# Kernel optimization log

Hardware: AMD Instinct MI355X
Metric: run time of the kernel (lower is better)

The kernel has to match this reference:

```python
import jax, jax.numpy as jnp
import numpy as np

B, S, T, H, E = 256, 512, 16, 1024, 512  # batch, src_len, trg_steps, hidden, emb_dim


def setup_inputs() -> dict:
    key = jax.random.key(0)
    ks = jax.random.split(key, 10)
    rn = lambda k, sh: jax.random.normal(k, sh, dtype=jnp.float32) * 0.05
    return {
        "trg_emb": rn(ks[0], (B, T, E)),
        "h0": rn(ks[1], (B, H)),
        "c0": rn(ks[2], (B, H)),
        "ctx": rn(ks[3], (B, S, H)),
        "src_len": jax.random.randint(ks[4], (B,), 1, S + 1, dtype=jnp.int32),
        "W_ih": rn(ks[5], (4 * H, E + H)),  # input-feeding: lstm in = emb + hidden
        "W_hh": rn(ks[6], (4 * H, H)),
        "b_ih": jnp.zeros((4 * H,), jnp.float32),
        "b_hh": jnp.zeros((4 * H,), jnp.float32),
        "W_in": rn(ks[7], (H, H)),    # attention linear_in (no bias)
        "W_out": rn(ks[8], (H, 2 * H)),  # attention linear_out (no bias)
    }


def reference(trg_emb, h0, c0, ctx, src_len, W_ih, W_hh, b_ih, b_hh, W_in, W_out):
    # mask[b, s] = s < src_len[b]
    mask = jnp.arange(S)[None, :] < src_len[:, None]  # (B, S)
    neg = jnp.float32(-1e9)

    def step(carry, emb_t):
        h, c, h_tilde = carry  # each (B, H); emb_t (B, E)
        # input feeding: concat target embedding with previous attentional vector
        x = jnp.concatenate([emb_t, h_tilde], axis=1)  # (B, E+H)
        gates = x @ W_ih.T + b_ih + h @ W_hh.T + b_hh  # (B, 4H), pytorch gate order i,f,g,o
        i, f, g, o = jnp.split(gates, 4, axis=1)
        i = jax.nn.sigmoid(i); f = jax.nn.sigmoid(f)
        g = jnp.tanh(g);       o = jax.nn.sigmoid(o)
        c = f * c + i * g
        h = o * jnp.tanh(c)
        # Luong soft-dot attention with src_len masking
        target = h @ W_in.T                                # (B, H)
        scores = jnp.einsum('bsh,bh->bs', ctx, target)     # (B, S)
        scores = jnp.where(mask, scores, neg)
        attn = jax.nn.softmax(scores, axis=-1)
        weighted = jnp.einsum('bs,bsh->bh', attn, ctx)     # (B, H)
        h_tilde = jnp.tanh(jnp.concatenate([weighted, h], axis=1) @ W_out.T)
        return (h, c, h_tilde), h_tilde

    # initial h_tilde = init_hidden[0] (per the original code)
    (h_f, c_f, _), hs = jax.lax.scan(step, (h0, c0, h0), jnp.swapaxes(trg_emb, 0, 1))
    output = jnp.swapaxes(hs, 0, 1)  # (B, T, H)
    return output, h_f, c_f
```

## Files before the change

kernel.cpp:

```cpp
#include <hip/hip_runtime.h>
#include <cstdint>
#include <cstddef>


#define B_ 256
#define S_ 512
#define T_ 16
#define H_ 1024
#define E_ 512
#define NBUF 4

typedef unsigned short u16;
using short8 = __attribute__((ext_vector_type(8))) short;
using f32x4  = __attribute__((ext_vector_type(4))) float;

__device__ __forceinline__ float bf2f(u16 u) {
  union { uint32_t i; float f; } v; v.i = ((uint32_t)u) << 16; return v.f;
}
__device__ __forceinline__ u16 f2bf(float f) {
  union { uint32_t i; float f; } v; v.f = f;
  uint32_t r = v.i + 0x7fffu + ((v.i >> 16) & 1u);
  return (u16)(r >> 16);
}
__device__ __forceinline__ ushort4 cvt4bf(float4 v) {
  ushort4 o; o.x = f2bf(v.x); o.y = f2bf(v.y); o.z = f2bf(v.z); o.w = f2bf(v.w);
  return o;
}
__device__ __forceinline__ float sigmoidf_(float x) { return 1.f / (1.f + __expf(-x)); }

__device__ __forceinline__ void gload_lds16(const void* g, void* l) {
  __builtin_amdgcn_global_load_lds(
      (const __attribute__((address_space(1))) void*)g,
      (__attribute__((address_space(3))) void*)l, 16, 0, 0);
}

struct Reg3 { const u16* A; int lda; const u16* B; int ldb; int kt; };

template <int EPI>
__global__ __launch_bounds__(128) void gemm_k(Reg3 r0, Reg3 r1, Reg3 r2,
                                              int nmb,
                                              float* __restrict__ Cf,
                                              u16* __restrict__ Cb,
                                              const float* __restrict__ bsum,
                                              float* __restrict__ cst,
                                              float* __restrict__ h32o,
                                              u16* __restrict__ hbfo,
                                              const int tstep) {
  __shared__ u16 smA[NBUF][64 * 64];
  __shared__ u16 smB[NBUF][64 * 64];
  const int tid = threadIdx.x;
  const int lane = tid & 63;
  const int wave = tid >> 6;
  const int m0 = (blockIdx.x % nmb) * 64;
  const int n0 = (blockIdx.x / nmb) * 64;
  const int row16 = lane & 15;
  const int kg = lane >> 4;
  const int nt = r0.kt + r1.kt + r2.kt;

  auto stage = [&](int ti, int buf) {
    const int k01 = r0.kt + r1.kt;
    const u16* Ap = (ti < r0.kt) ? r0.A : (ti < k01) ? r1.A : r2.A;
    const u16* Bp = (ti < r0.kt) ? r0.B : (ti < k01) ? r1.B : r2.B;
    const int lda = (ti < r0.kt) ? r0.lda : (ti < k01) ? r1.lda : r2.lda;
    const int ldb = (ti < r0.kt) ? r0.ldb : (ti < k01) ? r1.ldb : r2.ldb;
    const int base = (ti < r0.kt) ? 0 : (ti < k01) ? r0.kt : k01;
    const int kr = (ti - base) << 6;
#pragma unroll
    for (int j = 0; j < 4; ++j) {
      const int c = j * 128 + tid;
      const int row = c >> 3, q = c & 7;
      gload_lds16(Ap + (size_t)(m0 + row) * lda + kr + ((q ^ (row & 7)) << 3),
                  (char*)&smA[buf][0] + (size_t)(j * 128 + wave * 64) * 16);
    }
#pragma unroll
    for (int j = 0; j < 4; ++j) {
      const int c = j * 128 + tid;
      const int row = c >> 3, q = c & 7;
      gload_lds16(Bp + (size_t)(n0 + row) * ldb + kr + ((q ^ (row & 7)) << 3),
                  (char*)&smB[buf][0] + (size_t)(j * 128 + wave * 64) * 16);
    }
  };

  f32x4 acc[4][2] = {};
  stage(0, 0);
  if (nt > 1) stage(1, 1);
  for (int ti = 0; ti < nt; ++ti) {
    const int buf = ti & 3;
    if (ti + 2 < nt) {
      stage(ti + 2, (ti + 2) & 3);
      asm volatile("s_waitcnt vmcnt(16)" ::: "memory");
    } else if (ti + 1 < nt) {
      asm volatile("s_waitcnt vmcnt(8)" ::: "memory");
    } else {
      asm volatile("s_waitcnt vmcnt(0)" ::: "memory");
    }
    __builtin_amdgcn_s_barrier();
    __builtin_amdgcn_sched_barrier(0);
#pragma unroll
    for (int ks = 0; ks < 2; ++ks) {
      short8 af[4], bfr[2];
#pragma unroll
      for (int mi = 0; mi < 4; ++mi) {
        const int R = mi * 16 + row16;
        af[mi] = *(const short8*)((const char*)&smA[buf][0] +
                                  (size_t)(((R << 3) | ((ks * 4 + kg) ^ (R & 7))) << 4));
      }
#pragma unroll
      for (int ni = 0; ni < 2; ++ni) {
        const int R = wave * 32 + ni * 16 + row16;
        bfr[ni] = *(const short8*)((const char*)&smB[buf][0] +
                                   (size_t)(((R << 3) | ((ks * 4 + kg) ^ (R & 7))) << 4));
      }
      asm volatile("s_waitcnt lgkmcnt(0)" ::: "memory");
      __builtin_amdgcn_sched_barrier(0);
#pragma unroll
      for (int mi = 0; mi < 4; ++mi)
#pragma unroll
        for (int ni = 0; ni < 2; ++ni)
          acc[mi][ni] = __builtin_amdgcn_mfma_f32_16x16x32_bf16(af[mi], bfr[ni], acc[mi][ni], 0, 0, 0);
      __builtin_amdgcn_sched_barrier(0);
    }
  }
#pragma unroll
  for (int mi = 0; mi < 4; ++mi) {
#pragma unroll
    for (int ni = 0; ni < 2; ++ni) {
#pragma unroll
      for (int r = 0; r < 4; ++r) {
        const int row = m0 + mi * 16 + (kg << 2) + r;
        const int col = n0 + wave * 32 + ni * 16 + row16;
        float v = acc[mi][ni][r];
        if (EPI == 1) {
          Cb[row * H_ + col] = f2bf(v);
        } else if (EPI == 2) {
          float tv = tanhf(v);
          Cf[(size_t)row * (T_ * H_) + (size_t)tstep * H_ + col] = tv;
          Cb[row * H_ + col] = f2bf(tv);
        } else {
          v += bsum[col];
          float v1 = __shfl_xor(v, 1);
          float v2 = __shfl_xor(v, 2);
          float v3 = __shfl_xor(v, 3);
          if ((lane & 3) == 0) {
            const int u = col >> 2;
            float iv = sigmoidf_(v);
            float fv = sigmoidf_(v1);
            float gv = tanhf(v2);
            float ov = sigmoidf_(v3);
            float cn = fv * cst[row * H_ + u] + iv * gv;
            float hn = ov * tanhf(cn);
            cst[row * H_ + u] = cn;
            h32o[row * H_ + u] = hn;
            hbfo[row * H_ + u] = f2bf(hn);
          }
        }
      }
    }
  }
}

__device__ __forceinline__ int fidx(int lane, int j) {
  return (j << 6) + ((lane + (j << 2)) & 63);
}

__global__ __launch_bounds__(1024) void attn_k(const u16* __restrict__ tgt,
                                               const u16* __restrict__ ctxc,
                                               const int* __restrict__ offs,
                                               const int* __restrict__ src_len,
                                               u16* __restrict__ wwbf) {
  __shared__ float facc[8][1024];
  __shared__ float fm[16], fl[16];
  const int b = blockIdx.x;
  const int tid = threadIdx.x;
  const int lane = tid & 63;
  const int wave = tid >> 6;
  const int len = src_len[b];
  const u16* cb = ctxc + ((size_t)offs[b] << 10);

  float tg[16];
  {
    const u16* tp = tgt + b * H_ + lane * 16;
    short8 v1 = *(const short8*)tp;
    short8 v2 = *(const short8*)(tp + 8);
#pragma unroll
    for (int j = 0; j < 8; ++j) { tg[j] = bf2f((u16)v1[j]); tg[8 + j] = bf2f((u16)v2[j]); }
  }

  float m = -1e30f, l = 0.f;
  float acc[16];
#pragma unroll
  for (int j = 0; j < 16; ++j) acc[j] = 0.f;

  for (int s = wave; s < len; s += 16) {
    const u16* cr = cb + ((size_t)s << 10) + (lane << 4);
    short8 v1 = *(const short8*)cr;
    short8 v2 = *(const short8*)(cr + 8);
    float cf[16];
#pragma unroll
    for (int j = 0; j < 8; ++j) { cf[j] = bf2f((u16)v1[j]); cf[8 + j] = bf2f((u16)v2[j]); }
    float x = 0.f;
#pragma unroll
    for (int j = 0; j < 16; ++j) x += cf[j] * tg[j];
#pragma unroll
    for (int off = 1; off < 64; off <<= 1) x += __shfl_xor(x, off);
    if (x > m) {
      float sc_ = __expf(m - x);
      l *= sc_;
#pragma unroll
      for (int j = 0; j < 16; ++j) acc[j] *= sc_;
      m = x;
    }
    float p = __expf(x - m);
    l += p;
#pragma unroll
    for (int j = 0; j < 16; ++j) acc[j] += p * cf[j];
  }

  if (wave >= 8) {
#pragma unroll
    for (int j = 0; j < 16; ++j) facc[wave - 8][fidx(lane, j)] = acc[j];
    if (lane == 0) { fm[wave] = m; fl[wave] = l; }
  }
  __syncthreads();
  if (wave < 8) {
    float pm = fm[8 + wave];
    float pl = fl[8 + wave];
    float M = fmaxf(m, pm);
    float e1 = __expf(m - M);
    float e2 = __expf(pm - M);
#pragma unroll
    for (int j = 0; j < 16; ++j) {
      float pv = facc[wave][fidx(lane, j)];
      facc[wave][fidx(lane, j)] = acc[j] * e1 + pv * e2;
    }
    if (lane == 0) { fm[wave] = M; fl[wave] = l * e1 + pl * e2; }
  }
  __syncthreads();
  float mstar = -1e30f;
#pragma unroll
  for (int w = 0; w < 8; ++w) mstar = fmaxf(mstar, fm[w]);
  float lsum = 0.f, asum = 0.f;
  const int ri = fidx(tid >> 4, tid & 15);
#pragma unroll
  for (int w = 0; w < 8; ++w) {
    float e = __expf(fm[w] - mstar);
    lsum += fl[w] * e;
    asum += facc[w][ri] * e;
  }
  wwbf[b * H_ + tid] = f2bf(asum / lsum);
}

__global__ __launch_bounds__(256) void scan_k(const int* __restrict__ len,
                                              int* __restrict__ offs) {
  __shared__ int tmp[256];
  const int tid = threadIdx.x;
  const int v = len[tid];
  tmp[tid] = v;
  __syncthreads();
  for (int off = 1; off < 256; off <<= 1) {
    int t = (tid >= off) ? tmp[tid - off] : 0;
    __syncthreads();
    tmp[tid] += t;
    __syncthreads();
  }
  offs[tid] = tmp[tid] - v;
}

__global__ __launch_bounds__(256) void ctx_compact(const float* __restrict__ ctx,
                                                   const int* __restrict__ src_len,
                                                   const int* __restrict__ offs,
                                                   u16* __restrict__ ctxc) {
  const int b = blockIdx.x;
  const int n4 = src_len[b] << 8;
  const float4* s = (const float4*)(ctx + ((size_t)b << 19));
  ushort4* d = (ushort4*)(ctxc + ((size_t)offs[b] << 10));
  for (int i = threadIdx.x; i < n4; i += 256) d[i] = cvt4bf(s[i]);
}

__global__ __launch_bounds__(256) void convert_all(
    const float* __restrict__ W_ih, const float* __restrict__ W_hh,
    const float* __restrict__ W_in, const float* __restrict__ W_out,
    const float* __restrict__ trg_emb,
    const float* __restrict__ b_ih, const float* __restrict__ b_hh,
    const float* __restrict__ h0, const float* __restrict__ c0,
    u16* __restrict__ wWih, u16* __restrict__ wWhh, u16* __restrict__ wWin,
    u16* __restrict__ wWout, u16* __restrict__ wemb,
    float* __restrict__ wbsum, u16* __restrict__ wh0, u16* __restrict__ whtbf,
    float* __restrict__ wc) {
  const int gtid = blockIdx.x * 256 + threadIdx.x;
  const int GSZ = 1024 * 256;
  for (int i = gtid; i < 1572864; i += GSZ) {
    const int r = i / 384, c4 = i - r * 384;
    const int rp = ((r & 1023) << 2) + (r >> 10);
    ((ushort4*)wWih)[(size_t)rp * 384 + c4] = cvt4bf(((const float4*)W_ih)[i]);
  }
  for (int i = gtid; i < 1048576; i += GSZ) {
    const int r = i >> 8, c4 = i & 255;
    const int rp = ((r & 1023) << 2) + (r >> 10);
    ((ushort4*)wWhh)[(size_t)rp * 256 + c4] = cvt4bf(((const float4*)W_hh)[i]);
  }
  for (int i = gtid; i < 262144; i += GSZ)
    ((ushort4*)wWin)[i] = cvt4bf(((const float4*)W_in)[i]);
  for (int i = gtid; i < 524288; i += GSZ)
    ((ushort4*)wWout)[i] = cvt4bf(((const float4*)W_out)[i]);
  for (int i = gtid; i < 524288; i += GSZ)
    ((ushort4*)wemb)[i] = cvt4bf(((const float4*)trg_emb)[i]);
  if (gtid < 4096) {
    const int cp = ((gtid & 1023) << 2) + (gtid >> 10);
    wbsum[cp] = b_ih[gtid] + b_hh[gtid];
  }
  for (int i = gtid; i < 262144; i += GSZ) {
    u16 hb = f2bf(h0[i]);
    wh0[i] = hb;
    whtbf[i] = hb;
    wc[i] = c0[i];
  }
}

extern "C" void kernel_launch(void* const* d_in, const int* in_sizes, int n_in,
                              void* d_out, int out_size, void* d_ws, size_t ws_size,
                              hipStream_t stream) {
  const float* trg_emb = (const float*)d_in[0];
  const float* h0      = (const float*)d_in[1];
  const float* c0      = (const float*)d_in[2];
  const float* ctx     = (const float*)d_in[3];
  const int*   src_len = (const int*)d_in[4];
  const float* W_ih    = (const float*)d_in[5];
  const float* W_hh    = (const float*)d_in[6];
  const float* b_ih    = (const float*)d_in[7];
  const float* b_hh    = (const float*)d_in[8];
  const float* W_in    = (const float*)d_in[9];
  const float* W_out   = (const float*)d_in[10];
  float* out = (float*)d_out;

  char* w = (char*)d_ws;
  size_t off = 0;
  auto alloc = [&](size_t bytes) { char* p = w + off; off += bytes; return p; };
  u16*   wWih  = (u16*)  alloc(12582912);
  u16*   wWhh  = (u16*)  alloc(8388608);
  u16*   wWin  = (u16*)  alloc(2097152);
  u16*   wWout = (u16*)  alloc(4194304);
  u16*   wemb  = (u16*)  alloc(4194304);
  float* wbsum = (float*)alloc(16384);
  float* wh32  = (float*)alloc(1048576);
  float* wc    = (float*)alloc(1048576);
  u16*   wh0   = (u16*)  alloc(524288);
  u16*   wh1   = (u16*)  alloc(524288);
  u16*   whtbf = (u16*)  alloc(524288);
  u16*   wtgt  = (u16*)  alloc(524288);
  u16*   wwbf  = (u16*)  alloc(524288);
  int*   woffs = (int*)  alloc(1024);
  u16*   wctxc = (u16*)  alloc(268435456);
  (void)ws_size;

  scan_k<<<dim3(1), dim3(256), 0, stream>>>(src_len, woffs);
  convert_all<<<dim3(1024), dim3(256), 0, stream>>>(
      W_ih, W_hh, W_in, W_out, trg_emb, b_ih, b_hh, h0, c0,
      wWih, wWhh, wWin, wWout, wemb, wbsum, wh0, whtbf, wc);
  ctx_compact<<<dim3(B_), dim3(256), 0, stream>>>(ctx, src_len, woffs, wctxc);

  Reg3 rz = { nullptr, 0, nullptr, 0, 0 };
  for (int t = 0; t < T_; ++t) {
    const u16* hcur = (t & 1) ? wh1 : wh0;
    u16* hnxt = (t & 1) ? wh0 : wh1;
    Reg3 g0 = { wemb + (size_t)t * E_, T_ * E_, wWih,      E_ + H_, 8 };
    Reg3 g1 = { whtbf,                 H_,      wWih + E_, E_ + H_, 16 };
    Reg3 g2 = { hcur,                  H_,      wWhh,      H_,      16 };
    gemm_k<3><<<dim3(256), dim3(128), 0, stream>>>(
        g0, g1, g2, 4, nullptr, nullptr, wbsum, wc, wh32, hnxt, 0);
    Reg3 i0 = { hnxt, H_, wWin, H_, 16 };
    gemm_k<1><<<dim3(64), dim3(128), 0, stream>>>(
        i0, rz, rz, 4, nullptr, wtgt, nullptr, nullptr, nullptr, nullptr, 0);
    attn_k<<<dim3(B_), dim3(1024), 0, stream>>>(wtgt, wctxc, woffs, src_len, wwbf);
    Reg3 o0 = { wwbf, H_, wWout,      2 * H_, 16 };
    Reg3 o1 = { hnxt, H_, wWout + H_, 2 * H_, 16 };
    gemm_k<2><<<dim3(64), dim3(128), 0, stream>>>(
        o0, o1, rz, 4, out, whtbf, nullptr, nullptr, nullptr, nullptr, t);
  }
  hipMemcpyAsync(out + (size_t)B_ * T_ * H_, wh32, (size_t)B_ * H_ * sizeof(float),
                 hipMemcpyDeviceToDevice, stream);
  hipMemcpyAsync(out + (size_t)B_ * T_ * H_ + B_ * H_, wc, (size_t)B_ * H_ * sizeof(float),
                 hipMemcpyDeviceToDevice, stream);
}
```

Before: 2.096 ms.

## Split attention across block pairs, deepen GEMM pipeline, fuse setup kernels

The GEMM kernel now runs four waves in a 2x2 layout with a six-buffer, four-deep prefetch, so more waves share each 64x64 tile. Attention is split across two 512-thread blocks per batch row, each handling half the source positions. The two halves merge their online-softmax partials through a global flag handoff, and if the flag never arrives the first block processes the second half itself. The prefix scan and ctx compaction are folded into the conversion kernel, and the final h/c copies are replaced by writes from the last-step epilogue. This adds spin-wait synchronisation between blocks and reuses pacc across steps, which relies on stream ordering between launches.

Measured after the change: 1.914 ms. -8.7%, faster.

```diff
diff --git a/kernel.cpp b/kernel.cpp
--- a/kernel.cpp
+++ b/kernel.cpp
@@ -8,7 +8,7 @@
 #define T_ 16
 #define H_ 1024
 #define E_ 512
-#define NBUF 4
+#define NBUF 6
 
 typedef unsigned short u16;
 using short8 = __attribute__((ext_vector_type(8))) short;
@@ -37,20 +37,21 @@
 struct Reg3 { const u16* A; int lda; const u16* B; int ldb; int kt; };
 
 template <int EPI>
-__global__ __launch_bounds__(128) void gemm_k(Reg3 r0, Reg3 r1, Reg3 r2,
+__global__ __launch_bounds__(256) void gemm_k(Reg3 r0, Reg3 r1, Reg3 r2,
                                               int nmb,
                                               float* __restrict__ Cf,
                                               u16* __restrict__ Cb,
                                               const float* __restrict__ bsum,
                                               float* __restrict__ cst,
-                                              float* __restrict__ h32o,
                                               u16* __restrict__ hbfo,
+                                              float* __restrict__ outHC,
                                               const int tstep) {
-  __shared__ u16 smA[NBUF][64 * 64];
-  __shared__ u16 smB[NBUF][64 * 64];
+  __shared__ u16 smA[NBUF][4096];
+  __shared__ u16 smB[NBUF][4096];
   const int tid = threadIdx.x;
   const int lane = tid & 63;
   const int wave = tid >> 6;
+  const int wm = wave >> 1, wn = wave & 1;
   const int m0 = (blockIdx.x % nmb) * 64;
   const int n0 = (blockIdx.x / nmb) * 64;
   const int row16 = lane & 15;
@@ -66,31 +67,37 @@
     const int base = (ti < r0.kt) ? 0 : (ti < k01) ? r0.kt : k01;
     const int kr = (ti - base) << 6;
 #pragma unroll
-    for (int j = 0; j < 4; ++j) {
-      const int c = j * 128 + tid;
+    for (int j = 0; j < 2; ++j) {
+      const int c = j * 256 + tid;
       const int row = c >> 3, q = c & 7;
       gload_lds16(Ap + (size_t)(m0 + row) * lda + kr + ((q ^ (row & 7)) << 3),
-                  (char*)&smA[buf][0] + (size_t)(j * 128 + wave * 64) * 16);
-    }
-#pragma unroll
-    for (int j = 0; j < 4; ++j) {
-      const int c = j * 128 + tid;
+                  (char*)&smA[buf][0] + (size_t)(j * 256 + wave * 64) * 16);
+    }
+#pragma unroll
+    for (int j = 0; j < 2; ++j) {
+      const int c = j * 256 + tid;
       const int row = c >> 3, q = c & 7;
       gload_lds16(Bp + (size_t)(n0 + row) * ldb + kr + ((q ^ (row & 7)) << 3),
-                  (char*)&smB[buf][0] + (size_t)(j * 128 + wave * 64) * 16);
+                  (char*)&smB[buf][0] + (size_t)(j * 256 + wave * 64) * 16);
     }
   };
 
-  f32x4 acc[4][2] = {};
+  f32x4 acc[2][2] = {};
   stage(0, 0);
   if (nt > 1) stage(1, 1);
+  if (nt > 2) stage(2, 2);
+  if (nt > 3) stage(3, 3);
   for (int ti = 0; ti < nt; ++ti) {
-    const int buf = ti & 3;
-    if (ti + 2 < nt) {
-      stage(ti + 2, (ti + 2) & 3);
+    const int buf = ti % NBUF;
+    if (ti + 4 < nt) {
+      stage(ti + 4, (ti + 4) % NBUF);
       asm volatile("s_waitcnt vmcnt(16)" ::: "memory");
+    } else if (ti + 3 < nt) {
+      asm volatile("s_waitcnt vmcnt(12)" ::: "memory");
+    } else if (ti + 2 < nt) {
+      asm volatile("s_waitcnt vmcnt(8)" ::: "memory");
     } else if (ti + 1 < nt) {
-      asm volatile("s_waitcnt vmcnt(8)" ::: "memory");
+      asm volatile("s_waitcnt vmcnt(4)" ::: "memory");
     } else {
       asm volatile("s_waitcnt vmcnt(0)" ::: "memory");
     }
@@ -98,23 +105,23 @@
     __builtin_amdgcn_sched_barrier(0);
 #pragma unroll
     for (int ks = 0; ks < 2; ++ks) {
-      short8 af[4], bfr[2];
-#pragma unroll
-      for (int mi = 0; mi < 4; ++mi) {
-        const int R = mi * 16 + row16;
+      short8 af[2], bfr[2];
+#pragma unroll
+      for (int mi = 0; mi < 2; ++mi) {
+        const int R = wm * 32 + mi * 16 + row16;
         af[mi] = *(const short8*)((const char*)&smA[buf][0] +
                                   (size_t)(((R << 3) | ((ks * 4 + kg) ^ (R & 7))) << 4));
       }
 #pragma unroll
       for (int ni = 0; ni < 2; ++ni) {
-        const int R = wave * 32 + ni * 16 + row16;
+        const int R = wn * 32 + ni * 16 + row16;
         bfr[ni] = *(const short8*)((const char*)&smB[buf][0] +
                                    (size_t)(((R << 3) | ((ks * 4 + kg) ^ (R & 7))) << 4));
       }
       asm volatile("s_waitcnt lgkmcnt(0)" ::: "memory");
       __builtin_amdgcn_sched_barrier(0);
 #pragma unroll
-      for (int mi = 0; mi < 4; ++mi)
+      for (int mi = 0; mi < 2; ++mi)
 #pragma unroll
         for (int ni = 0; ni < 2; ++ni)
           acc[mi][ni] = __builtin_amdgcn_mfma_f32_16x16x32_bf16(af[mi], bfr[ni], acc[mi][ni], 0, 0, 0);
@@ -122,13 +129,13 @@
     }
   }
 #pragma unroll
-  for (int mi = 0; mi < 4; ++mi) {
+  for (int mi = 0; mi < 2; ++mi) {
 #pragma unroll
     for (int ni = 0; ni < 2; ++ni) {
 #pragma unroll
       for (int r = 0; r < 4; ++r) {
-        const int row = m0 + mi * 16 + (kg << 2) + r;
-        const int col = n0 + wave * 32 + ni * 16 + row16;
+        const int row = m0 + wm * 32 + mi * 16 + (kg << 2) + r;
+        const int col = n0 + wn * 32 + ni * 16 + row16;
         float v = acc[mi][ni][r];
         if (EPI == 1) {
           Cb[row * H_ + col] = f2bf(v);
@@ -150,8 +157,11 @@
             float cn = fv * cst[row * H_ + u] + iv * gv;
             float hn = ov * tanhf(cn);
             cst[row * H_ + u] = cn;
-            h32o[row * H_ + u] = hn;
             hbfo[row * H_ + u] = f2bf(hn);
+            if (outHC) {
+              outHC[row * H_ + u] = hn;
+              outHC[B_ * H_ + row * H_ + u] = cn;
+            }
           }
         }
       }
@@ -163,35 +173,39 @@
   return (j << 6) + ((lane + (j << 2)) & 63);
 }
 
-__global__ __launch_bounds__(1024) void attn_k(const u16* __restrict__ tgt,
-                                               const u16* __restrict__ ctxc,
-                                               const int* __restrict__ offs,
-                                               const int* __restrict__ src_len,
-                                               u16* __restrict__ wwbf) {
-  __shared__ float facc[8][1024];
-  __shared__ float fm[16], fl[16];
-  const int b = blockIdx.x;
+__global__ __launch_bounds__(512, 4) void attn_pair(const u16* __restrict__ tgt,
+                                                    const u16* __restrict__ ctxc,
+                                                    const int* __restrict__ woffs,
+                                                    const int* __restrict__ src_len,
+                                                    u16* __restrict__ wwbf,
+                                                    float* __restrict__ pacc,
+                                                    float* __restrict__ pml,
+                                                    int* __restrict__ flag) {
+  __shared__ float facc[7][1024];
+  __shared__ float fm[8], fl[8];
+  const int p = blockIdx.x >> 1;
+  const int half = blockIdx.x & 1;
   const int tid = threadIdx.x;
   const int lane = tid & 63;
   const int wave = tid >> 6;
-  const int len = src_len[b];
-  const u16* cb = ctxc + ((size_t)offs[b] << 10);
+  const int len = src_len[p];
+  const int len2 = (len + 1) >> 1;
+  const u16* cb = ctxc + ((size_t)woffs[p] << 10);
 
   float tg[16];
   {
-    const u16* tp = tgt + b * H_ + lane * 16;
+    const u16* tp = tgt + p * H_ + lane * 16;
     short8 v1 = *(const short8*)tp;
     short8 v2 = *(const short8*)(tp + 8);
 #pragma unroll
     for (int j = 0; j < 8; ++j) { tg[j] = bf2f((u16)v1[j]); tg[8 + j] = bf2f((u16)v2[j]); }
   }
-
   float m = -1e30f, l = 0.f;
   float acc[16];
 #pragma unroll
   for (int j = 0; j < 16; ++j) acc[j] = 0.f;
 
-  for (int s = wave; s < len; s += 16) {
+  auto process = [&](int s) {
     const u16* cr = cb + ((size_t)s << 10) + (lane << 4);
     short8 v1 = *(const short8*)cr;
     short8 v2 = *(const short8*)(cr + 8);
@@ -210,84 +224,102 @@
       for (int j = 0; j < 16; ++j) acc[j] *= sc_;
       m = x;
     }
-    float p = __expf(x - m);
-    l += p;
-#pragma unroll
-    for (int j = 0; j < 16; ++j) acc[j] += p * cf[j];
-  }
-
-  if (wave >= 8) {
-#pragma unroll
-    for (int j = 0; j < 16; ++j) facc[wave - 8][fidx(lane, j)] = acc[j];
+    float pv = __expf(x - m);
+    l += pv;
+#pragma unroll
+    for (int j = 0; j < 16; ++j) acc[j] += pv * cf[j];
+  };
+
+  const int lo = half ? len2 : 0;
+  const int hi = half ? len : len2;
+  for (int s = lo + wave; s < hi; s += 8) process(s);
+
+  if (wave >= 1) {
+#pragma unroll
+    for (int j = 0; j < 16; ++j) facc[wave - 1][fidx(lane, j)] = acc[j];
     if (lane == 0) { fm[wave] = m; fl[wave] = l; }
   }
   __syncthreads();
-  if (wave < 8) {
-    float pm = fm[8 + wave];
-    float pl = fl[8 + wave];
-    float M = fmaxf(m, pm);
-    float e1 = __expf(m - M);
-    float e2 = __expf(pm - M);
-#pragma unroll
-    for (int j = 0; j < 16; ++j) {
-      float pv = facc[wave][fidx(lane, j)];
-      facc[wave][fidx(lane, j)] = acc[j] * e1 + pv * e2;
-    }
-    if (lane == 0) { fm[wave] = M; fl[wave] = l * e1 + pl * e2; }
-  }
-  __syncthreads();
-  float mstar = -1e30f;
-#pragma unroll
-  for (int w = 0; w < 8; ++w) mstar = fmaxf(mstar, fm[w]);
-  float lsum = 0.f, asum = 0.f;
-  const int ri = fidx(tid >> 4, tid & 15);
-#pragma unroll
-  for (int w = 0; w < 8; ++w) {
-    float e = __expf(fm[w] - mstar);
-    lsum += fl[w] * e;
-    asum += facc[w][ri] * e;
-  }
-  wwbf[b * H_ + tid] = f2bf(asum / lsum);
-}
-
-__global__ __launch_bounds__(256) void scan_k(const int* __restrict__ len,
-                                              int* __restrict__ offs) {
-  __shared__ int tmp[256];
-  const int tid = threadIdx.x;
-  const int v = len[tid];
-  tmp[tid] = v;
-  __syncthreads();
-  for (int off = 1; off < 256; off <<= 1) {
-    int t = (tid >= off) ? tmp[tid - off] : 0;
-    __syncthreads();
-    tmp[tid] += t;
-    __syncthreads();
-  }
-  offs[tid] = tmp[tid] - v;
-}
-
-__global__ __launch_bounds__(256) void ctx_compact(const float* __restrict__ ctx,
-                                                   const int* __restrict__ src_len,
-                                                   const int* __restrict__ offs,
-                                                   u16* __restrict__ ctxc) {
-  const int b = blockIdx.x;
-  const int n4 = src_len[b] << 8;
-  const float4* s = (const float4*)(ctx + ((size_t)b << 19));
-  ushort4* d = (ushort4*)(ctxc + ((size_t)offs[b] << 10));
-  for (int i = threadIdx.x; i < n4; i += 256) d[i] = cvt4bf(s[i]);
+  if (wave == 0) {
+#pragma unroll
+    for (int w = 1; w < 8; ++w) {
+      float pm2 = fm[w], pl2 = fl[w];
+      float M = fmaxf(m, pm2);
+      float e1 = __expf(m - M), e2 = __expf(pm2 - M);
+#pragma unroll
+      for (int j = 0; j < 16; ++j)
+        acc[j] = acc[j] * e1 + facc[w - 1][fidx(lane, j)] * e2;
+      l = l * e1 + pl2 * e2;
+      m = M;
+    }
+    if (half == 1) {
+      float* pa = pacc + (size_t)p * 1024;
+#pragma unroll
+      for (int j4 = 0; j4 < 4; ++j4) {
+        float4 v;
+        v.x = acc[j4 * 4]; v.y = acc[j4 * 4 + 1];
+        v.z = acc[j4 * 4 + 2]; v.w = acc[j4 * 4 + 3];
+        *(float4*)&pa[lane * 16 + j4 * 4] = v;
+      }
+      if (lane == 0) { pml[2 * p] = m; pml[2 * p + 1] = l; }
+      asm volatile("s_waitcnt vmcnt(0)" ::: "memory");
+      if (lane == 0)
+        __hip_atomic_store(flag + p, 1, __ATOMIC_RELEASE, __HIP_MEMORY_SCOPE_AGENT);
+    } else {
+      int got = 0;
+      if (lane == 0) {
+        for (unsigned c2 = 0; c2 < (1u << 10); ++c2) {
+          if (__hip_atomic_load(flag + p, __ATOMIC_RELAXED, __HIP_MEMORY_SCOPE_AGENT) != 0) {
+            got = 1; break;
+          }
+          __builtin_amdgcn_s_sleep(2);
+        }
+        if (got)
+          (void)__hip_atomic_load(flag + p, __ATOMIC_ACQUIRE, __HIP_MEMORY_SCOPE_AGENT);
+      }
+      got = __shfl(got, 0);
+      if (got) {
+        const float* pa = pacc + (size_t)p * 1024;
+        float pm2 = pml[2 * p], pl2 = pml[2 * p + 1];
+        float M = fmaxf(m, pm2);
+        float e1 = __expf(m - M), e2 = __expf(pm2 - M);
+#pragma unroll
+        for (int j = 0; j < 16; ++j)
+          acc[j] = acc[j] * e1 + pa[lane * 16 + j] * e2;
+        l = l * e1 + pl2 * e2;
+        m = M;
+      } else {
+        for (int s = len2; s < len; ++s) process(s);
+      }
+      const float inv = 1.f / l;
+#pragma unroll
+      for (int j4 = 0; j4 < 4; ++j4) {
+        ushort4 o;
+        o.x = f2bf(acc[j4 * 4] * inv);
+        o.y = f2bf(acc[j4 * 4 + 1] * inv);
+        o.z = f2bf(acc[j4 * 4 + 2] * inv);
+        o.w = f2bf(acc[j4 * 4 + 3] * inv);
+        *(ushort4*)(wwbf + p * H_ + lane * 16 + j4 * 4) = o;
+      }
+    }
+  }
 }
 
 __global__ __launch_bounds__(256) void convert_all(
     const float* __restrict__ W_ih, const float* __restrict__ W_hh,
     const float* __restrict__ W_in, const float* __restrict__ W_out,
-    const float* __restrict__ trg_emb,
+    const float* __restrict__ trg_emb, const float* __restrict__ ctx,
     const float* __restrict__ b_ih, const float* __restrict__ b_hh,
     const float* __restrict__ h0, const float* __restrict__ c0,
+    const int* __restrict__ src_len,
     u16* __restrict__ wWih, u16* __restrict__ wWhh, u16* __restrict__ wWin,
     u16* __restrict__ wWout, u16* __restrict__ wemb,
     float* __restrict__ wbsum, u16* __restrict__ wh0, u16* __restrict__ whtbf,
-    float* __restrict__ wc) {
-  const int gtid = blockIdx.x * 256 + threadIdx.x;
+    float* __restrict__ wc, int* __restrict__ woffs, u16* __restrict__ ctxc) {
+  __shared__ int tmp[256];
+  const int bid = blockIdx.x;
+  const int tid = threadIdx.x;
+  const int gtid = bid * 256 + tid;
   const int GSZ = 1024 * 256;
   for (int i = gtid; i < 1572864; i += GSZ) {
     const int r = i / 384, c4 = i - r * 384;
@@ -314,6 +346,21 @@
     wh0[i] = hb;
     whtbf[i] = hb;
     wc[i] = c0[i];
+  }
+  if (bid >= 768) {
+    const int b = bid - 768;
+    tmp[tid] = (tid < b) ? src_len[tid] : 0;
+    __syncthreads();
+    for (int o = 128; o > 0; o >>= 1) {
+      if (tid < o) tmp[tid] += tmp[tid + o];
+      __syncthreads();
+    }
+    const int off = tmp[0];
+    if (tid == 0) woffs[b] = off;
+    const int n4 = src_len[b] << 8;
+    const float4* s = (const float4*)(ctx + ((size_t)b << 19));
+    ushort4* d = (ushort4*)(ctxc + ((size_t)off << 10));
+    for (int i = tid; i < n4; i += 256) d[i] = cvt4bf(s[i]);
   }
 }
 
@@ -342,7 +389,6 @@
   u16*   wWout = (u16*)  alloc(4194304);
   u16*   wemb  = (u16*)  alloc(4194304);
   float* wbsum = (float*)alloc(16384);
-  float* wh32  = (float*)alloc(1048576);
   float* wc    = (float*)alloc(1048576);
   u16*   wh0   = (u16*)  alloc(524288);
   u16*   wh1   = (u16*)  alloc(524288);
@@ -350,14 +396,16 @@
   u16*   wtgt  = (u16*)  alloc(524288);
   u16*   wwbf  = (u16*)  alloc(524288);
   int*   woffs = (int*)  alloc(1024);
+  int*   wflag = (int*)  alloc(16384);
+  float* pacc  = (float*)alloc(1048576);
+  float* pml   = (float*)alloc(2048);
   u16*   wctxc = (u16*)  alloc(268435456);
   (void)ws_size;
 
-  scan_k<<<dim3(1), dim3(256), 0, stream>>>(src_len, woffs);
+  hipMemsetAsync(wflag, 0, 16384, stream);
   convert_all<<<dim3(1024), dim3(256), 0, stream>>>(
-      W_ih, W_hh, W_in, W_out, trg_emb, b_ih, b_hh, h0, c0,
-      wWih, wWhh, wWin, wWout, wemb, wbsum, wh0, whtbf, wc);
-  ctx_compact<<<dim3(B_), dim3(256), 0, stream>>>(ctx, src_len, woffs, wctxc);
+      W_ih, W_hh, W_in, W_out, trg_emb, ctx, b_ih, b_hh, h0, c0, src_len,
+      wWih, wWhh, wWin, wWout, wemb, wbsum, wh0, whtbf, wc, woffs, wctxc);
 
   Reg3 rz = { nullptr, 0, nullptr, 0, 0 };
   for (int t = 0; t < T_; ++t) {
@@ -366,19 +414,17 @@
     Reg3 g0 = { wemb + (size_t)t * E_, T_ * E_, wWih,      E_ + H_, 8 };
     Reg3 g1 = { whtbf,                 H_,      wWih + E_, E_ + H_, 16 };
     Reg3 g2 = { hcur,                  H_,      wWhh,      H_,      16 };
-    gemm_k<3><<<dim3(256), dim3(128), 0, stream>>>(
-        g0, g1, g2, 4, nullptr, nullptr, wbsum, wc, wh32, hnxt, 0);
+    gemm_k<3><<<dim3(256), dim3(256), 0, stream>>>(
+        g0, g1, g2, 4, nullptr, nullptr, wbsum, wc, hnxt,
+        (t == T_ - 1) ? out + (size_t)B_ * T_ * H_ : nullptr, 0);
     Reg3 i0 = { hnxt, H_, wWin, H_, 16 };
-    gemm_k<1><<<dim3(64), dim3(128), 0, stream>>>(
+    gemm_k<1><<<dim3(64), dim3(256), 0, stream>>>(
         i0, rz, rz, 4, nullptr, wtgt, nullptr, nullptr, nullptr, nullptr, 0);
-    attn_k<<<dim3(B_), dim3(1024), 0, stream>>>(wtgt, wctxc, woffs, src_len, wwbf);
+    attn_pair<<<dim3(512), dim3(512), 0, stream>>>(
+        wtgt, wctxc, woffs, src_len, wwbf, pacc, pml, wflag + t * 256);
     Reg3 o0 = { wwbf, H_, wWout,      2 * H_, 16 };
     Reg3 o1 = { hnxt, H_, wWout + H_, 2 * H_, 16 };
-    gemm_k<2><<<dim3(64), dim3(128), 0, stream>>>(
+    gemm_k<2><<<dim3(64), dim3(256), 0, stream>>>(
         o0, o1, rz, 4, out, whtbf, nullptr, nullptr, nullptr, nullptr, t);
   }
-  hipMemcpyAsync(out + (size_t)B_ * T_ * H_, wh32, (size_t)B_ * H_ * sizeof(float),
-                 hipMemcpyDeviceToDevice, stream);
-  hipMemcpyAsync(out + (size_t)B_ * T_ * H_ + B_ * H_, wc, (size_t)B_ * H_ * sizeof(float),
-                 hipMemcpyDeviceToDevice, stream);
-}
+}
```
